# Kernel tuning notes

Measured on AMD Instinct MI355X. Metric: run time of the kernel, lower is better.

Reference implementation:

```python
import jax, jax.numpy as jnp
import numpy as np

B, T, H = 1024, 512, 256  # batch, seq_len, hidden_layer_size; input_size=1, output_size=1


def setup_inputs() -> dict:
    key = jax.random.key(0)
    ks = jax.random.split(key, 7)
    s = 1.0 / np.sqrt(H)  # PyTorch LSTM/Linear init scale (uniform bound); normal here, scaled similarly
    return {
        "input_seq": jax.random.normal(ks[0], (B, T), dtype=jnp.float32),
        "W_ih": jax.random.normal(ks[1], (4 * H, 1), dtype=jnp.float32) * s,
        "W_hh": jax.random.normal(ks[2], (4 * H, H), dtype=jnp.float32) * s,
        "b_ih": jax.random.normal(ks[3], (4 * H,), dtype=jnp.float32) * s,
        "b_hh": jax.random.normal(ks[4], (4 * H,), dtype=jnp.float32) * s,
        "W_lin": jax.random.normal(ks[5], (1, H), dtype=jnp.float32) * s,
        "b_lin": jax.random.normal(ks[6], (1,), dtype=jnp.float32) * s,
    }


def _lstm_last_hidden(x, W_ih, W_hh, b_ih, b_hh):
    # x: [B, T] scalar series -> treated as [B, T, 1] (input_size = 1).
    # Precompute the input projection for all timesteps at once:
    # xg[b, t, :] = x[b, t] * W_ih[:, 0] + b_ih + b_hh   -> [B, T, 4H]
    xg = x[:, :, None] * W_ih[:, 0] + (b_ih + b_hh)
    xg = jnp.swapaxes(xg, 0, 1)  # [T, B, 4H] for scan over time

    h0 = jnp.zeros((x.shape[0], H), dtype=x.dtype)
    c0 = jnp.zeros((x.shape[0], H), dtype=x.dtype)

    def step(carry, xg_t):
        h, c = carry
        gates = xg_t + h @ W_hh.T  # [B, 4H]
        i, f, g, o = jnp.split(gates, 4, axis=-1)  # PyTorch gate order: i, f, g, o
        i = jax.nn.sigmoid(i)
        f = jax.nn.sigmoid(f)
        g = jnp.tanh(g)
        o = jax.nn.sigmoid(o)
        c = f * c + i * g
        h = o * jnp.tanh(c)
        return (h, c), None

    (h_n, _), _ = jax.lax.scan(step, (h0, c0), xg)
    return h_n  # [B, H]


def reference(input_seq, W_ih, W_hh, b_ih, b_hh, W_lin, b_lin):
    h_n = _lstm_last_hidden(input_seq, W_ih, W_hh, b_ih, b_hh)
    predictions = h_n @ W_lin.T + b_lin  # [B, 1]
    return predictions
```

## Files before the change

kernel.cpp:

```cpp
#include <hip/hip_runtime.h>


#define HID 256
#define TT 512
#define NBLK 64
#define THREADS 512
#define HPAD 264

typedef float v4f __attribute__((ext_vector_type(4)));
typedef unsigned int v4u __attribute__((ext_vector_type(4)));
typedef __bf16 v8bf __attribute__((ext_vector_type(8)));

__device__ __forceinline__ unsigned short f2bf(float f) {
    unsigned int u = __builtin_bit_cast(unsigned int, f);
    u += 0x7fffu + ((u >> 16) & 1u);
    return (unsigned short)(u >> 16);
}
__device__ __forceinline__ float bf2f(unsigned short s) {
    unsigned int u = ((unsigned int)s) << 16;
    return __builtin_bit_cast(float, u);
}
__device__ __forceinline__ float fsigmoid(float x) {
    float e = exp2f(x * -1.44269504f);
    return __builtin_amdgcn_rcpf(1.0f + e);
}
__device__ __forceinline__ float ftanh(float x) {
    float e = exp2f(x * 2.88539008f);
    return 1.0f - 2.0f * __builtin_amdgcn_rcpf(1.0f + e);
}

__global__ void wconv_kernel(const float* __restrict__ Whh,
                             unsigned short* __restrict__ Wbf) {
    int tid = blockIdx.x * blockDim.x + threadIdx.x;
    int lane = tid & 63;
    int frag = tid >> 6;
    int Tn = frag >> 3;
    int kc = frag & 7;
    int n  = Tn * 16 + (lane & 15);
    int kb = kc * 32 + (lane >> 4) * 8;
    const float* src = Whh + (size_t)n * HID + kb;
    unsigned short* dst = Wbf + (size_t)tid * 8;
#pragma unroll
    for (int j = 0; j < 8; ++j) dst[j] = f2bf(src[j]);
}

#define MFMA_BF16 __builtin_amdgcn_mfma_f32_16x16x32_bf16

__global__ __launch_bounds__(THREADS, 1)
void lstm_kernel(const float* __restrict__ x,
                 const float* __restrict__ W_ih,
                 const float* __restrict__ b_ih,
                 const float* __restrict__ b_hh,
                 const float* __restrict__ W_lin,
                 const float* __restrict__ b_lin,
                 const unsigned short* __restrict__ Wbf,
                 float* __restrict__ out) {
    __shared__ __align__(16) unsigned short Wlds[16 * 8 * 64 * 8];
    __shared__ __align__(16) unsigned short hbuf[2][16 * HPAD];
    __shared__ __align__(16) float cpk[2048];
    __shared__ float part[THREADS];

    const int tid  = threadIdx.x;
    const int lane = tid & 63;
    const int w    = tid >> 6;
    const int l4   = lane & 15;
    const int quad = lane >> 4;
    const int r0   = blockIdx.x * 16;

#pragma unroll
    for (int S = 0; S < 2; ++S) {
        int Tn = 32 + w + 8 * S;
        int slot = w * 2 + S;
#pragma unroll
        for (int kc = 0; kc < 8; ++kc)
            *(v4u*)(Wlds + ((size_t)((slot * 8 + kc) * 64 + lane)) * 8) =
                *(const v4u*)(Wbf + ((size_t)((Tn * 8 + kc) * 64 + lane)) * 8);
    }

    for (int i = tid; i < 2048; i += THREADS) {
        int col = i >> 3, j = i & 7;
        cpk[i] = (j < 4) ? W_ih[j * 256 + col]
                         : b_ih[(j - 4) * 256 + col] + b_hh[(j - 4) * 256 + col];
    }

    for (int i = tid; i < 16 * HPAD; i += THREADS) hbuf[0][i] = 0;

    v8bf wr[2][3][8];
#pragma unroll
    for (int S = 0; S < 2; ++S)
#pragma unroll
        for (int G = 0; G < 3; ++G) {
            int gc = (G == 2) ? 3 : G;
            int Tn = 16 * gc + w + 8 * S;
#pragma unroll
            for (int kc = 0; kc < 8; ++kc)
                wr[S][G][kc] = __builtin_bit_cast(v8bf, *(const v4u*)(Wbf +
                    ((size_t)(Tn * 8 + kc) * 64 + lane) * 8));
        }

    float xv[4];
#pragma unroll
    for (int r = 0; r < 4; ++r) xv[r] = x[(size_t)(r0 + quad * 4 + r) * TT];

    __syncthreads();

    float c_st[8];
#pragma unroll
    for (int i = 0; i < 8; ++i) c_st[i] = 0.0f;
    int cur = 0;

    for (int t = 0; t < TT; ++t) {
        const unsigned short* hrow = hbuf[cur] + l4 * HPAD + quad * 8;
        unsigned short* hn = hbuf[cur ^ 1];

        v4f ai0 = 0.f, af0 = 0.f, ao0 = 0.f, ag0 = 0.f;
        v4f ai1 = 0.f, af1 = 0.f, ao1 = 0.f, ag1 = 0.f;

#pragma unroll
        for (int kc = 0; kc < 8; ++kc) {
            v8bf a = __builtin_bit_cast(v8bf, *(const v4u*)(hrow + kc * 32));
            v8bf g0 = __builtin_bit_cast(v8bf, *(const v4u*)(Wlds +
                        ((size_t)(((w * 2 + 0) * 8 + kc) * 64 + lane)) * 8));
            v8bf g1 = __builtin_bit_cast(v8bf, *(const v4u*)(Wlds +
                        ((size_t)(((w * 2 + 1) * 8 + kc) * 64 + lane)) * 8));
            ai0 = MFMA_BF16(a, wr[0][0][kc], ai0, 0, 0, 0);
            af0 = MFMA_BF16(a, wr[0][1][kc], af0, 0, 0, 0);
            ao0 = MFMA_BF16(a, wr[0][2][kc], ao0, 0, 0, 0);
            ag0 = MFMA_BF16(a, g0, ag0, 0, 0, 0);
            ai1 = MFMA_BF16(a, wr[1][0][kc], ai1, 0, 0, 0);
            af1 = MFMA_BF16(a, wr[1][1][kc], af1, 0, 0, 0);
            ao1 = MFMA_BF16(a, wr[1][2][kc], ao1, 0, 0, 0);
            ag1 = MFMA_BF16(a, g1, ag1, 0, 0, 0);
        }

        {
            int colS = 16 * w + l4;
            v4f w4 = *(const v4f*)(cpk + colS * 8);
            v4f b4 = *(const v4f*)(cpk + colS * 8 + 4);
#pragma unroll
            for (int r = 0; r < 4; ++r) {
                float gi = fsigmoid(ai0[r] + xv[r] * w4[0] + b4[0]);
                float gf = fsigmoid(af0[r] + xv[r] * w4[1] + b4[1]);
                float gg = ftanh(ag0[r] + xv[r] * w4[2] + b4[2]);
                float go = fsigmoid(ao0[r] + xv[r] * w4[3] + b4[3]);
                float cn = gf * c_st[r] + gi * gg;
                c_st[r] = cn;
                hn[(quad * 4 + r) * HPAD + colS] = f2bf(go * ftanh(cn));
            }
        }
        {
            int colS = 16 * (w + 8) + l4;
            v4f w4 = *(const v4f*)(cpk + colS * 8);
            v4f b4 = *(const v4f*)(cpk + colS * 8 + 4);
#pragma unroll
            for (int r = 0; r < 4; ++r) {
                float gi = fsigmoid(ai1[r] + xv[r] * w4[0] + b4[0]);
                float gf = fsigmoid(af1[r] + xv[r] * w4[1] + b4[1]);
                float gg = ftanh(ag1[r] + xv[r] * w4[2] + b4[2]);
                float go = fsigmoid(ao1[r] + xv[r] * w4[3] + b4[3]);
                float cn = gf * c_st[4 + r] + gi * gg;
                c_st[4 + r] = cn;
                hn[(quad * 4 + r) * HPAD + colS] = f2bf(go * ftanh(cn));
            }
        }

        {
            int tn = (t + 1) & (TT - 1);
#pragma unroll
            for (int r = 0; r < 4; ++r)
                xv[r] = x[(size_t)(r0 + quad * 4 + r) * TT + tn];
        }

        __syncthreads();
        cur ^= 1;
    }

    {
        int rrow = tid >> 5, s5 = tid & 31;
        float p = 0.0f;
#pragma unroll
        for (int jj = 0; jj < 8; ++jj) {
            int j = s5 * 8 + jj;
            p += bf2f(hbuf[cur][rrow * HPAD + j]) * W_lin[j];
        }
        part[tid] = p;
    }
    __syncthreads();
    if (tid < 16) {
        float sum = 0.0f;
#pragma unroll
        for (int s = 0; s < 32; ++s) sum += part[tid * 32 + s];
        out[r0 + tid] = sum + b_lin[0];
    }
}

extern "C" void kernel_launch(void* const* d_in, const int* in_sizes, int n_in,
                              void* d_out, int out_size, void* d_ws, size_t ws_size,
                              hipStream_t stream) {
    const float* x     = (const float*)d_in[0];
    const float* W_ih  = (const float*)d_in[1];
    const float* W_hh  = (const float*)d_in[2];
    const float* b_ih  = (const float*)d_in[3];
    const float* b_hh  = (const float*)d_in[4];
    const float* W_lin = (const float*)d_in[5];
    const float* b_lin = (const float*)d_in[6];
    unsigned short* Wbf = (unsigned short*)d_ws;

    wconv_kernel<<<128, 256, 0, stream>>>(W_hh, Wbf);
    lstm_kernel<<<NBLK, THREADS, 0, stream>>>(x, W_ih, b_ih, b_hh, W_lin, b_lin,
                                              Wbf, (float*)d_out);
}
```

Before: 1.814 ms.

## Replace per-step block barrier with per-wave LDS flags and triple-buffered hidden state

Drops the __syncthreads at the end of every timestep. Each wave now publishes its finished hidden-state chunk through an LDS flag, and consumers spin-wait only on the K-chunk they need next. Each wave starts with its own chunk in a rotated order, and a third h buffer prevents write-after-read hazards between steps. Column ownership is changed to contiguous 32-column chunks, and the o-gate weights are streamed from global memory per step instead of held in registers to relieve register pressure. The spin-wait correctness relies on the LDS ordering given by the lgkmcnt wait, and the extra global loads could add latency.

```diff
diff --git a/kernel.cpp b/kernel.cpp
--- a/kernel.cpp
+++ b/kernel.cpp
@@ -56,9 +56,8 @@
                  const unsigned short* __restrict__ Wbf,
                  float* __restrict__ out) {
     __shared__ __align__(16) unsigned short Wlds[16 * 8 * 64 * 8];
-    __shared__ __align__(16) unsigned short hbuf[2][16 * HPAD];
-    __shared__ __align__(16) float cpk[2048];
-    __shared__ float part[THREADS];
+    __shared__ __align__(16) unsigned short hbuf[3][16 * HPAD];
+    __shared__ int flags[16];
 
     const int tid  = threadIdx.x;
     const int lane = tid & 63;
@@ -66,37 +65,52 @@
     const int l4   = lane & 15;
     const int quad = lane >> 4;
     const int r0   = blockIdx.x * 16;
-
-#pragma unroll
-    for (int S = 0; S < 2; ++S) {
-        int Tn = 32 + w + 8 * S;
-        int slot = w * 2 + S;
+    const int colA = 32 * w + l4;
+    const int colB = 32 * w + 16 + l4;
+
+#pragma unroll
+    for (int ct = 0; ct < 2; ++ct)
 #pragma unroll
         for (int kc = 0; kc < 8; ++kc)
-            *(v4u*)(Wlds + ((size_t)((slot * 8 + kc) * 64 + lane)) * 8) =
-                *(const v4u*)(Wbf + ((size_t)((Tn * 8 + kc) * 64 + lane)) * 8);
-    }
-
-    for (int i = tid; i < 2048; i += THREADS) {
-        int col = i >> 3, j = i & 7;
-        cpk[i] = (j < 4) ? W_ih[j * 256 + col]
-                         : b_ih[(j - 4) * 256 + col] + b_hh[(j - 4) * 256 + col];
+            *(v4u*)(Wlds + ((size_t)(((2 * w + ct) * 8 + kc) * 64 + lane)) * 8) =
+                *(const v4u*)(Wbf +
+                    ((size_t)(((32 + 2 * w + ct) * 8 + kc) * 64 + lane)) * 8);
+
+    v8bf wif[2][2][8];
+#pragma unroll
+    for (int G = 0; G < 2; ++G)
+#pragma unroll
+        for (int ct = 0; ct < 2; ++ct) {
+            int Tn = 16 * G + 2 * w + ct;
+#pragma unroll
+            for (int idx = 0; idx < 8; ++idx) {
+                int kc = (w + idx) & 7;
+                wif[G][ct][idx] = __builtin_bit_cast(v8bf, *(const v4u*)(Wbf +
+                    ((size_t)(Tn * 8 + kc) * 64 + lane) * 8));
+            }
+        }
+
+    const v4u* optA = (const v4u*)Wbf + ((size_t)(48 + 2 * w) * 8) * 64 + lane;
+    const v4u* optB = optA + (size_t)8 * 64;
+    v4u obA[4], obB[4];
+#pragma unroll
+    for (int j = 0; j < 4; ++j) {
+        int kcj = (w + j) & 7;
+        obA[j] = optA[kcj * 64];
+        obB[j] = optB[kcj * 64];
+    }
+
+    float cw[2][4], cb[2][4];
+#pragma unroll
+    for (int g = 0; g < 4; ++g) {
+        cw[0][g] = W_ih[g * 256 + colA];
+        cb[0][g] = b_ih[g * 256 + colA] + b_hh[g * 256 + colA];
+        cw[1][g] = W_ih[g * 256 + colB];
+        cb[1][g] = b_ih[g * 256 + colB] + b_hh[g * 256 + colB];
     }
 
     for (int i = tid; i < 16 * HPAD; i += THREADS) hbuf[0][i] = 0;
-
-    v8bf wr[2][3][8];
-#pragma unroll
-    for (int S = 0; S < 2; ++S)
-#pragma unroll
-        for (int G = 0; G < 3; ++G) {
-            int gc = (G == 2) ? 3 : G;
-            int Tn = 16 * gc + w + 8 * S;
-#pragma unroll
-            for (int kc = 0; kc < 8; ++kc)
-                wr[S][G][kc] = __builtin_bit_cast(v8bf, *(const v4u*)(Wbf +
-                    ((size_t)(Tn * 8 + kc) * 64 + lane) * 8));
-        }
+    if (tid < 16) flags[tid] = 0;
 
     float xv[4];
 #pragma unroll
@@ -107,62 +121,64 @@
     float c_st[8];
 #pragma unroll
     for (int i = 0; i < 8; ++i) c_st[i] = 0.0f;
-    int cur = 0;
-
+
+    int cs = 0;
     for (int t = 0; t < TT; ++t) {
-        const unsigned short* hrow = hbuf[cur] + l4 * HPAD + quad * 8;
-        unsigned short* hn = hbuf[cur ^ 1];
-
-        v4f ai0 = 0.f, af0 = 0.f, ao0 = 0.f, ag0 = 0.f;
-        v4f ai1 = 0.f, af1 = 0.f, ao1 = 0.f, ag1 = 0.f;
-
-#pragma unroll
-        for (int kc = 0; kc < 8; ++kc) {
-            v8bf a = __builtin_bit_cast(v8bf, *(const v4u*)(hrow + kc * 32));
+        int ns = (cs == 2) ? 0 : cs + 1;
+        const unsigned short* hb = hbuf[cs] + l4 * HPAD + quad * 8;
+        unsigned short* hn = hbuf[ns];
+
+        v4f acc[2][4];
+#pragma unroll
+        for (int ct = 0; ct < 2; ++ct)
+#pragma unroll
+            for (int g = 0; g < 4; ++g) acc[ct][g] = 0.f;
+
+#pragma unroll
+        for (int idx = 0; idx < 8; ++idx) {
+            int rk = (w + idx) & 7;
+            if (idx != 0) {
+                volatile int* vf = (volatile int*)flags;
+                while (vf[rk] < t) __builtin_amdgcn_s_sleep(1);
+                asm volatile("" ::: "memory");
+            }
+            v8bf a  = __builtin_bit_cast(v8bf, *(const v4u*)(hb + rk * 32));
             v8bf g0 = __builtin_bit_cast(v8bf, *(const v4u*)(Wlds +
-                        ((size_t)(((w * 2 + 0) * 8 + kc) * 64 + lane)) * 8));
+                        ((size_t)(((2 * w + 0) * 8 + rk) * 64 + lane)) * 8));
             v8bf g1 = __builtin_bit_cast(v8bf, *(const v4u*)(Wlds +
-                        ((size_t)(((w * 2 + 1) * 8 + kc) * 64 + lane)) * 8));
-            ai0 = MFMA_BF16(a, wr[0][0][kc], ai0, 0, 0, 0);
-            af0 = MFMA_BF16(a, wr[0][1][kc], af0, 0, 0, 0);
-            ao0 = MFMA_BF16(a, wr[0][2][kc], ao0, 0, 0, 0);
-            ag0 = MFMA_BF16(a, g0, ag0, 0, 0, 0);
-            ai1 = MFMA_BF16(a, wr[1][0][kc], ai1, 0, 0, 0);
-            af1 = MFMA_BF16(a, wr[1][1][kc], af1, 0, 0, 0);
-            ao1 = MFMA_BF16(a, wr[1][2][kc], ao1, 0, 0, 0);
-            ag1 = MFMA_BF16(a, g1, ag1, 0, 0, 0);
-        }
-
-        {
-            int colS = 16 * w + l4;
-            v4f w4 = *(const v4f*)(cpk + colS * 8);
-            v4f b4 = *(const v4f*)(cpk + colS * 8 + 4);
+                        ((size_t)(((2 * w + 1) * 8 + rk) * 64 + lane)) * 8));
+            acc[0][0] = MFMA_BF16(a, wif[0][0][idx], acc[0][0], 0, 0, 0);
+            acc[1][0] = MFMA_BF16(a, wif[0][1][idx], acc[1][0], 0, 0, 0);
+            acc[0][1] = MFMA_BF16(a, wif[1][0][idx], acc[0][1], 0, 0, 0);
+            acc[1][1] = MFMA_BF16(a, wif[1][1][idx], acc[1][1], 0, 0, 0);
+            acc[0][2] = MFMA_BF16(a, g0, acc[0][2], 0, 0, 0);
+            acc[1][2] = MFMA_BF16(a, g1, acc[1][2], 0, 0, 0);
+            acc[0][3] = MFMA_BF16(a, __builtin_bit_cast(v8bf, obA[idx & 3]),
+                                  acc[0][3], 0, 0, 0);
+            acc[1][3] = MFMA_BF16(a, __builtin_bit_cast(v8bf, obB[idx & 3]),
+                                  acc[1][3], 0, 0, 0);
+            int pk = (w + idx + 4) & 7;
+            obA[idx & 3] = optA[pk * 64];
+            obB[idx & 3] = optB[pk * 64];
+        }
+
+#pragma unroll
+        for (int ct = 0; ct < 2; ++ct) {
+            int col = (ct == 0) ? colA : colB;
 #pragma unroll
             for (int r = 0; r < 4; ++r) {
-                float gi = fsigmoid(ai0[r] + xv[r] * w4[0] + b4[0]);
-                float gf = fsigmoid(af0[r] + xv[r] * w4[1] + b4[1]);
-                float gg = ftanh(ag0[r] + xv[r] * w4[2] + b4[2]);
-                float go = fsigmoid(ao0[r] + xv[r] * w4[3] + b4[3]);
-                float cn = gf * c_st[r] + gi * gg;
-                c_st[r] = cn;
-                hn[(quad * 4 + r) * HPAD + colS] = f2bf(go * ftanh(cn));
+                float gi = fsigmoid(acc[ct][0][r] + xv[r] * cw[ct][0] + cb[ct][0]);
+                float gf = fsigmoid(acc[ct][1][r] + xv[r] * cw[ct][1] + cb[ct][1]);
+                float gg = ftanh(acc[ct][2][r] + xv[r] * cw[ct][2] + cb[ct][2]);
+                float go = fsigmoid(acc[ct][3][r] + xv[r] * cw[ct][3] + cb[ct][3]);
+                float cn = gf * c_st[ct * 4 + r] + gi * gg;
+                c_st[ct * 4 + r] = cn;
+                hn[(quad * 4 + r) * HPAD + col] = f2bf(go * ftanh(cn));
             }
         }
-        {
-            int colS = 16 * (w + 8) + l4;
-            v4f w4 = *(const v4f*)(cpk + colS * 8);
-            v4f b4 = *(const v4f*)(cpk + colS * 8 + 4);
-#pragma unroll
-            for (int r = 0; r < 4; ++r) {
-                float gi = fsigmoid(ai1[r] + xv[r] * w4[0] + b4[0]);
-                float gf = fsigmoid(af1[r] + xv[r] * w4[1] + b4[1]);
-                float gg = ftanh(ag1[r] + xv[r] * w4[2] + b4[2]);
-                float go = fsigmoid(ao1[r] + xv[r] * w4[3] + b4[3]);
-                float cn = gf * c_st[4 + r] + gi * gg;
-                c_st[4 + r] = cn;
-                hn[(quad * 4 + r) * HPAD + colS] = f2bf(go * ftanh(cn));
-            }
-        }
+
+        asm volatile("s_waitcnt lgkmcnt(0)" ::: "memory");
+        if (lane == 0) *(volatile int*)&flags[w] = t + 1;
 
         {
             int tn = (t + 1) & (TT - 1);
@@ -170,18 +186,19 @@
             for (int r = 0; r < 4; ++r)
                 xv[r] = x[(size_t)(r0 + quad * 4 + r) * TT + tn];
         }
-
-        __syncthreads();
-        cur ^= 1;
-    }
-
+        cs = ns;
+    }
+
+    __syncthreads();
+
+    float* part = (float*)Wlds;
     {
         int rrow = tid >> 5, s5 = tid & 31;
         float p = 0.0f;
 #pragma unroll
         for (int jj = 0; jj < 8; ++jj) {
             int j = s5 * 8 + jj;
-            p += bf2f(hbuf[cur][rrow * HPAD + j]) * W_lin[j];
+            p += bf2f(hbuf[cs][rrow * HPAD + j]) * W_lin[j];
         }
         part[tid] = p;
     }
```

Result: slower. 2.770 ms (+52.7%).
